# Performance work log

Measured on AMD Instinct MI355X. Metric: run time of the kernel, lower is better.

## Reference

```python
import jax, jax.numpy as jnp
import numpy as np

B, S, D = 2, 2048, 2048
NQ, NKV = 16, 4
HD = D // NQ           # 128
GROUP = NQ // NKV      # 4


def setup_inputs() -> dict:
    key = jax.random.key(0)
    k_x, k_q, k_k, k_v, k_o = jax.random.split(key, 5)
    scale = 0.02
    return {
        "x": jax.random.normal(k_x, (B, S, D), dtype=jnp.float32),
        # torch nn.Linear weights have shape (out_features, in_features)
        "Wq": jax.random.normal(k_q, (D, D), dtype=jnp.float32) * scale,
        "Wk": jax.random.normal(k_k, (NKV * HD, D), dtype=jnp.float32) * scale,
        "Wv": jax.random.normal(k_v, (NKV * HD, D), dtype=jnp.float32) * scale,
        "Wo": jax.random.normal(k_o, (D, D), dtype=jnp.float32) * scale,
    }


def reference(x, Wq, Wk, Wv, Wo):
    b, s, _ = x.shape
    # projections (Linear: x @ W.T), then split heads -> (b, h, s, hd)
    Q = (x @ Wq.T).reshape(b, s, NQ, HD).transpose(0, 2, 1, 3)
    K = (x @ Wk.T).reshape(b, s, NKV, HD).transpose(0, 2, 1, 3)
    V = (x @ Wv.T).reshape(b, s, NKV, HD).transpose(0, 2, 1, 3)
    # GQA: broadcast each KV head across its query-head group (repeat_interleave on head dim)
    K = jnp.repeat(K, GROUP, axis=1)  # (b, NQ, s, hd)
    V = jnp.repeat(V, GROUP, axis=1)
    scores = jnp.einsum("bhqd,bhkd->bhqk", Q, K) / jnp.sqrt(jnp.float32(HD))
    causal = jnp.triu(jnp.ones((s, s), dtype=bool), k=1)  # True above diagonal -> masked
    scores = jnp.where(causal, -jnp.inf, scores)
    weights = jax.nn.softmax(scores, axis=-1)  # dropout p=0.0 -> identity
    ctx = jnp.einsum("bhqk,bhkd->bhqd", weights, V)
    ctx = ctx.transpose(0, 2, 1, 3).reshape(b, s, D)
    return ctx @ Wo.T
```

## Files before the change

kernel.cpp:

```cpp
#include <hip/hip_runtime.h>
#include <stdint.h>

#define S_LEN 2048
#define DMODEL 2048
#define NQH 16
#define NKVH 4
#define HDK 128

typedef __bf16 bf16x8 __attribute__((ext_vector_type(8)));
typedef float f32x4 __attribute__((ext_vector_type(4)));
typedef float f32x16 __attribute__((ext_vector_type(16)));

__device__ __forceinline__ void async16(const void* g, void* l) {
  __builtin_amdgcn_global_load_lds((const __attribute__((address_space(1))) void*)g,
                                   (__attribute__((address_space(3))) void*)l,
                                   16, 0, 0);
}

__device__ __forceinline__ f32x4 mfma16(bf16x8 a, bf16x8 b, f32x4 c) {
  return __builtin_amdgcn_mfma_f32_16x16x32_bf16(a, b, c, 0, 0, 0);
}
__device__ __forceinline__ f32x16 mfma32(bf16x8 a, bf16x8 b, f32x16 c) {
  return __builtin_amdgcn_mfma_f32_32x32x16_bf16(a, b, c, 0, 0, 0);
}
__device__ __forceinline__ uint32_t pkbf16(float lo, float hi) {
  uint32_t r;
  asm("v_cvt_pk_bf16_f32 %0, %1, %2" : "=v"(r) : "v"(lo), "v"(hi));
  return r;
}

__global__ __launch_bounds__(256) void cvt_bf16(const float* __restrict__ in,
                                                __bf16* __restrict__ out, int n) {
  int i = (blockIdx.x * 256 + threadIdx.x) * 8;
  if (i >= n) return;
  const float4* p = (const float4*)(in + i);
  float4 a = p[0], b = p[1];
  bf16x8 o;
  o[0] = (__bf16)a.x; o[1] = (__bf16)a.y; o[2] = (__bf16)a.z; o[3] = (__bf16)a.w;
  o[4] = (__bf16)b.x; o[5] = (__bf16)b.y; o[6] = (__bf16)b.z; o[7] = (__bf16)b.w;
  *(bf16x8*)(out + i) = o;
}

template <bool F32OUT>
__global__ __launch_bounds__(256) void gemm_bt(const __bf16* __restrict__ A,
                                               const __bf16* __restrict__ Ba,
                                               const __bf16* __restrict__ Bb,
                                               void* __restrict__ Ca,
                                               void* __restrict__ Cb,
                                               int M, int Ntot, int Nsplit, int K) {
  int nbn = Ntot >> 7;
  int bx = blockIdx.x;
  int m0 = (bx / nbn) << 7;
  int n0g = (bx % nbn) << 7;
  const __bf16* B;
  void* C;
  int n0, Nc;
  if (n0g < Nsplit) { B = Ba; C = Ca; n0 = n0g; Nc = Nsplit; }
  else              { B = Bb; C = Cb; n0 = n0g - Nsplit; Nc = Ntot - Nsplit; }

  __shared__ __align__(16) uint8_t As[16384];
  __shared__ __align__(16) uint8_t Bs[16384];

  int t = threadIdx.x, lane = t & 63, w = t >> 6;
  int wr = w >> 1, wc = w & 1;
  f32x4 acc[4][4] = {};

  for (int k0 = 0; k0 < K; k0 += 64) {
#pragma unroll
    for (int i = 0; i < 4; ++i) {
      int c = (i << 8) + t;
      int row = c >> 3;
      int colb = ((c & 7) << 4) ^ ((row & 7) << 4);
      async16((const uint8_t*)(A + (size_t)(m0 + row) * K + k0) + colb, As + c * 16);
      async16((const uint8_t*)(B + (size_t)(n0 + row) * K + k0) + colb, Bs + c * 16);
    }
    __syncthreads();
#pragma unroll
    for (int ks = 0; ks < 2; ++ks) {
      bf16x8 af[4], bfr[4];
#pragma unroll
      for (int m = 0; m < 4; ++m) {
        int row = wr * 64 + m * 16 + (lane & 15);
        int colb = ((ks << 6) + ((lane >> 4) << 4)) ^ ((row & 7) << 4);
        af[m] = *(const bf16x8*)(As + row * 128 + colb);
      }
#pragma unroll
      for (int n = 0; n < 4; ++n) {
        int row = wc * 64 + n * 16 + (lane & 15);
        int colb = ((ks << 6) + ((lane >> 4) << 4)) ^ ((row & 7) << 4);
        bfr[n] = *(const bf16x8*)(Bs + row * 128 + colb);
      }
      __builtin_amdgcn_s_setprio(1);
#pragma unroll
      for (int m = 0; m < 4; ++m)
#pragma unroll
        for (int n = 0; n < 4; ++n)
          acc[m][n] = mfma16(af[m], bfr[n], acc[m][n]);
      __builtin_amdgcn_s_setprio(0);
    }
    __syncthreads();
  }
#pragma unroll
  for (int m = 0; m < 4; ++m)
#pragma unroll
    for (int n = 0; n < 4; ++n)
#pragma unroll
      for (int j = 0; j < 4; ++j) {
        int mg = m0 + wr * 64 + m * 16 + ((lane >> 4) << 2) + j;
        int ng = n0 + wc * 64 + n * 16 + (lane & 15);
        float v = acc[m][n][j];
        if (F32OUT) ((float*)C)[(size_t)mg * Nc + ng] = v;
        else        ((__bf16*)C)[(size_t)mg * Nc + ng] = (__bf16)v;
      }
}

__global__ __launch_bounds__(256) void transpose_v(const __bf16* __restrict__ V,
                                                   __bf16* __restrict__ Vt) {
  int bid = blockIdx.x;
  int dt = bid & 1, st = (bid >> 1) & 31, kvh = (bid >> 6) & 3, b = bid >> 8;
  __shared__ __align__(16) __bf16 tile[64][72];
  int t = threadIdx.x;
#pragma unroll
  for (int i = 0; i < 2; ++i) {
    int c = (i << 8) + t;
    int sr = c >> 3, cb = (c & 7) << 3;
    bf16x8 v = *(const bf16x8*)(V + (size_t)(b * S_LEN + st * 64 + sr) * 512 +
                                kvh * HDK + dt * 64 + cb);
    *(bf16x8*)(&tile[sr][cb]) = v;
  }
  __syncthreads();
#pragma unroll
  for (int i = 0; i < 2; ++i) {
    int c = (i << 8) + t;
    int dr = c >> 3, sb = (c & 7) << 3;
    bf16x8 o;
#pragma unroll
    for (int j = 0; j < 8; ++j) o[j] = tile[sb + j][dr];
    *(bf16x8*)(Vt + (size_t)((b * NKVH + kvh) * HDK + dt * 64 + dr) * S_LEN +
               st * 64 + sb) = o;
  }
}

__global__ __launch_bounds__(256, 2) void attn(const __bf16* __restrict__ Q,
                                               const __bf16* __restrict__ Kx,
                                               const __bf16* __restrict__ Vt,
                                               __bf16* __restrict__ Ctx) {
  int bid = blockIdx.x;
  int qt = 15 - (bid & 15);
  int h = (bid >> 4) & 15;
  int b = bid >> 8;
  int kvh = h >> 2;
  int q0 = qt << 7;
  int t = threadIdx.x, lane = t & 63, w = t >> 6;
  int qr = lane & 31;
  int hi = lane >> 5;
  int qwb = q0 + (w << 5);

  __shared__ __align__(16) uint8_t Ks[2][16384];
  __shared__ __align__(16) uint8_t Vs[2][16384];

  const __bf16* kbase = Kx + (size_t)b * S_LEN * 512 + kvh * HDK;
  const __bf16* vbase = Vt + (size_t)(b * NKVH + kvh) * HDK * S_LEN;

  auto stage = [&](int kt, int bufi) {
#pragma unroll
    for (int i = 0; i < 4; ++i) {
      int c = (i << 8) + t;
      int krow = c >> 4;
      int kcolb = ((c & 15) << 4) ^ ((krow & 7) << 4);
      async16((const uint8_t*)(kbase + (size_t)((kt << 6) + krow) * 512) + kcolb,
              Ks[bufi] + c * 16);
      int vrow = c >> 3;
      int vcolb = ((c & 7) << 4) ^ ((vrow & 7) << 4);
      async16((const uint8_t*)(vbase + (size_t)vrow * S_LEN + (kt << 6)) + vcolb,
              Vs[bufi] + c * 16);
    }
  };

  int NT = (qt << 1) + 2;
  stage(0, 0);

  bf16x8 qf[8];
  {
    const __bf16* qrow = Q + (size_t)(b * S_LEN + qwb + qr) * DMODEL + h * HDK + hi * 8;
#pragma unroll
    for (int dk = 0; dk < 8; ++dk) qf[dk] = *(const bf16x8*)(qrow + dk * 16);
  }
  __syncthreads();

  const float NEG = -3.0e38f;
  const float SC = 0.08838834764831845f;
  float m_run = NEG, l_run = 0.f;
  f32x16 acc[4] = {};

  for (int kt = 0; kt < NT; ++kt) {
    int cur = kt & 1;
    if (kt + 1 < NT) stage(kt + 1, cur ^ 1);
    int k0 = kt << 6;
    if (k0 <= qwb + 31) {
      const uint8_t* ks = Ks[cur];
      const uint8_t* vs = Vs[cur];

      f32x16 st0 = {}, st1 = {};
      __builtin_amdgcn_s_setprio(1);
#pragma unroll
      for (int dk = 0; dk < 8; ++dk) {
        int cb = (dk << 5) + (hi << 4);
        int swz = (qr & 7) << 4;
        bf16x8 kf0 = *(const bf16x8*)(ks + qr * 256 + (cb ^ swz));
        st0 = mfma32(kf0, qf[dk], st0);
        bf16x8 kf1 = *(const bf16x8*)(ks + (32 + qr) * 256 + (cb ^ swz));
        st1 = mfma32(kf1, qf[dk], st1);
      }
      __builtin_amdgcn_s_setprio(0);

      if (k0 + 63 > qwb) {
#pragma unroll
        for (int r = 0; r < 16; ++r) {
          int kl = (r & 3) + ((r >> 2) << 3) + (hi << 2);
          st0[r] = (k0 + kl > qwb + qr) ? NEG : st0[r];
          st1[r] = (k0 + 32 + kl > qwb + qr) ? NEG : st1[r];
        }
      }

      float mx = fmaxf(st0[0], st1[0]);
#pragma unroll
      for (int r = 1; r < 16; ++r) mx = fmaxf(mx, fmaxf(st0[r], st1[r]));
      mx = fmaxf(mx, __shfl_xor(mx, 32, 64));

      if (__any(mx > m_run + 90.52f)) {
        float mn = fmaxf(m_run, mx);
        float al = __expf((m_run - mn) * SC);
        l_run *= al;
        m_run = mn;
#pragma unroll
        for (int i = 0; i < 16; ++i) {
          float alr = __shfl(al, (i & 3) + ((i >> 2) << 3) + (hi << 2), 64);
          acc[0][i] *= alr; acc[1][i] *= alr; acc[2][i] *= alr; acc[3][i] *= alr;
        }
      }

      float mSC = m_run * SC;
      float rs = 0.f;
      float p0[16], p1[16];
#pragma unroll
      for (int r = 0; r < 16; ++r) { p0[r] = __expf(fmaf(st0[r], SC, -mSC)); rs += p0[r]; }
#pragma unroll
      for (int r = 0; r < 16; ++r) { p1[r] = __expf(fmaf(st1[r], SC, -mSC)); rs += p1[r]; }
      rs += __shfl_xor(rs, 32, 64);
      l_run += rs;

      uint32_t wd0[4][2], wd1[4][2];
#pragma unroll
      for (int g = 0; g < 4; ++g) {
        wd0[g][0] = pkbf16(p0[4 * g + 0], p0[4 * g + 1]);
        wd0[g][1] = pkbf16(p0[4 * g + 2], p0[4 * g + 3]);
        wd1[g][0] = pkbf16(p1[4 * g + 0], p1[4 * g + 1]);
        wd1[g][1] = pkbf16(p1[4 * g + 2], p1[4 * g + 3]);
      }
      bf16x8 pa[4];
#define PEXCH(WD, IDX0, IDX1)                                                  \
      {                                                                        \
        uint32_t s0 = hi ? WD[0][0] : WD[1][0];                                \
        uint32_t s1 = hi ? WD[0][1] : WD[1][1];                                \
        uint32_t s2 = hi ? WD[2][0] : WD[3][0];                                \
        uint32_t s3 = hi ? WD[2][1] : WD[3][1];                                \
        uint32_t r0 = (uint32_t)__shfl_xor((int)s0, 32, 64);                   \
        uint32_t r1 = (uint32_t)__shfl_xor((int)s1, 32, 64);                   \
        uint32_t r2 = (uint32_t)__shfl_xor((int)s2, 32, 64);                   \
        uint32_t r3 = (uint32_t)__shfl_xor((int)s3, 32, 64);                   \
        union { bf16x8 v; uint32_t u[4]; } fa, fb;                             \
        fa.u[0] = hi ? r0 : WD[0][0];                                          \
        fa.u[1] = hi ? r1 : WD[0][1];                                          \
        fa.u[2] = hi ? WD[1][0] : r0;                                          \
        fa.u[3] = hi ? WD[1][1] : r1;                                          \
        fb.u[0] = hi ? r2 : WD[2][0];                                          \
        fb.u[1] = hi ? r3 : WD[2][1];                                          \
        fb.u[2] = hi ? WD[3][0] : r2;                                          \
        fb.u[3] = hi ? WD[3][1] : r3;                                          \
        pa[IDX0] = fa.v;                                                       \
        pa[IDX1] = fb.v;                                                       \
      }
      PEXCH(wd0, 0, 1)
      PEXCH(wd1, 2, 3)
#undef PEXCH

      __builtin_amdgcn_s_setprio(1);
#pragma unroll
      for (int dt = 0; dt < 4; ++dt) {
        int row = (dt << 5) + qr;
        int swz = (row & 7) << 4;
#pragma unroll
        for (int kc = 0; kc < 4; ++kc) {
          bf16x8 vf = *(const bf16x8*)(vs + row * 128 + (((kc << 5) + (hi << 4)) ^ swz));
          acc[dt] = mfma32(pa[kc], vf, acc[dt]);
        }
      }
      __builtin_amdgcn_s_setprio(0);
    }
    __syncthreads();
  }

#pragma unroll
  for (int i = 0; i < 16; ++i) {
    int rm = (i & 3) + ((i >> 2) << 3) + (hi << 2);
    float lr = __shfl(l_run, rm, 64);
    float inv = 1.0f / lr;
    size_t rowoff = (size_t)(b * S_LEN + qwb + rm) * DMODEL + h * HDK + qr;
#pragma unroll
    for (int dt = 0; dt < 4; ++dt)
      Ctx[rowoff + (dt << 5)] = (__bf16)(acc[dt][i] * inv);
  }
}

extern "C" void kernel_launch(void* const* d_in, const int* in_sizes, int n_in,
                              void* d_out, int out_size, void* d_ws, size_t ws_size,
                              hipStream_t stream) {
  const float* x  = (const float*)d_in[0];
  const float* Wq = (const float*)d_in[1];
  const float* Wk = (const float*)d_in[2];
  const float* Wv = (const float*)d_in[3];
  const float* Wo = (const float*)d_in[4];
  float* out = (float*)d_out;

  const size_t MB = 1024 * 1024;
  uint8_t* ws = (uint8_t*)d_ws;
  __bf16* xb  = (__bf16*)(ws + 0 * MB);
  __bf16* Wqb = (__bf16*)(ws + 16 * MB);
  __bf16* Wkb = (__bf16*)(ws + 24 * MB);
  __bf16* Wvb = (__bf16*)(ws + 26 * MB);
  __bf16* Wob = (__bf16*)(ws + 28 * MB);
  __bf16* Qb  = (__bf16*)(ws + 36 * MB);
  __bf16* Kb  = (__bf16*)(ws + 52 * MB);
  __bf16* Vb  = (__bf16*)(ws + 56 * MB);
  __bf16* Vtb = (__bf16*)(ws + 60 * MB);
  __bf16* Ctx = (__bf16*)(ws + 64 * MB);

  cvt_bf16<<<8388608 / 2048, 256, 0, stream>>>(x, xb, 8388608);
  cvt_bf16<<<4194304 / 2048, 256, 0, stream>>>(Wq, Wqb, 4194304);
  cvt_bf16<<<1048576 / 2048, 256, 0, stream>>>(Wk, Wkb, 1048576);
  cvt_bf16<<<1048576 / 2048, 256, 0, stream>>>(Wv, Wvb, 1048576);
  cvt_bf16<<<4194304 / 2048, 256, 0, stream>>>(Wo, Wob, 4194304);

  gemm_bt<false><<<(4096 / 128) * (2048 / 128), 256, 0, stream>>>(
      xb, Wqb, Wqb, (void*)Qb, (void*)Qb, 4096, 2048, 2048, 2048);
  gemm_bt<false><<<(4096 / 128) * (1024 / 128), 256, 0, stream>>>(
      xb, Wkb, Wvb, (void*)Kb, (void*)Vb, 4096, 1024, 512, 2048);

  transpose_v<<<512, 256, 0, stream>>>(Vb, Vtb);

  attn<<<2 * 16 * 16, 256, 0, stream>>>(Qb, Kb, Vtb, Ctx);

  gemm_bt<true><<<(4096 / 128) * (2048 / 128), 256, 0, stream>>>(
      Ctx, Wob, Wob, (void*)out, (void*)out, 4096, 2048, 2048, 2048);
}
```

Baseline: 233.2 us.

## Fuse conversions and QKV GEMMs, add XCD-aware block remap, tree reductions

Merges the five fp32-to-bf16 conversion launches into one kernel, and the Q and K/V projection GEMMs into a single launch with three output splits. It also remaps block indices in the GEMMs and the attention kernel so that neighbouring tiles are spread across the XCDs. The softmax max and sum reductions inside attention become tree reductions to shorten dependency chains. The aim is to cut launch overhead and tail effects and to improve L2 locality, at the cost of extra branching and index arithmetic.

```diff
diff --git a/kernel.cpp b/kernel.cpp
--- a/kernel.cpp
+++ b/kernel.cpp
@@ -29,10 +29,22 @@
   return r;
 }
 
-__global__ __launch_bounds__(256) void cvt_bf16(const float* __restrict__ in,
-                                                __bf16* __restrict__ out, int n) {
-  int i = (blockIdx.x * 256 + threadIdx.x) * 8;
-  if (i >= n) return;
+__global__ __launch_bounds__(256) void cvt_all(
+    const float* __restrict__ i0, const float* __restrict__ i1,
+    const float* __restrict__ i2, const float* __restrict__ i3,
+    const float* __restrict__ i4, __bf16* __restrict__ o0,
+    __bf16* __restrict__ o1, __bf16* __restrict__ o2, __bf16* __restrict__ o3,
+    __bf16* __restrict__ o4) {
+  int v = blockIdx.x * 256 + threadIdx.x;
+  const float* in;
+  __bf16* out;
+  int base;
+  if (v < 1048576)      { in = i0; out = o0; base = 0; }
+  else if (v < 1572864) { in = i1; out = o1; base = 1048576; }
+  else if (v < 1703936) { in = i2; out = o2; base = 1572864; }
+  else if (v < 1835008) { in = i3; out = o3; base = 1703936; }
+  else                  { in = i4; out = o4; base = 1835008; }
+  int i = (v - base) * 8;
   const float4* p = (const float4*)(in + i);
   float4 a = p[0], b = p[1];
   bf16x8 o;
@@ -43,20 +55,25 @@
 
 template <bool F32OUT>
 __global__ __launch_bounds__(256) void gemm_bt(const __bf16* __restrict__ A,
-                                               const __bf16* __restrict__ Ba,
-                                               const __bf16* __restrict__ Bb,
-                                               void* __restrict__ Ca,
-                                               void* __restrict__ Cb,
-                                               int M, int Ntot, int Nsplit, int K) {
+                                               const __bf16* __restrict__ B0,
+                                               const __bf16* __restrict__ B1,
+                                               const __bf16* __restrict__ B2,
+                                               void* __restrict__ C0,
+                                               void* __restrict__ C1,
+                                               void* __restrict__ C2,
+                                               int Ntot, int Ns1, int Ns2, int K) {
   int nbn = Ntot >> 7;
-  int bx = blockIdx.x;
+  int nwg = gridDim.x;
+  int bid = blockIdx.x;
+  int bx = (bid & 7) * (nwg >> 3) + (bid >> 3);
   int m0 = (bx / nbn) << 7;
   int n0g = (bx % nbn) << 7;
   const __bf16* B;
   void* C;
   int n0, Nc;
-  if (n0g < Nsplit) { B = Ba; C = Ca; n0 = n0g; Nc = Nsplit; }
-  else              { B = Bb; C = Cb; n0 = n0g - Nsplit; Nc = Ntot - Nsplit; }
+  if (n0g < Ns1)      { B = B0; C = C0; n0 = n0g;       Nc = Ns1; }
+  else if (n0g < Ns2) { B = B1; C = C1; n0 = n0g - Ns1; Nc = Ns2 - Ns1; }
+  else                { B = B2; C = C2; n0 = n0g - Ns2; Nc = Ntot - Ns2; }
 
   __shared__ __align__(16) uint8_t As[16384];
   __shared__ __align__(16) uint8_t Bs[16384];
@@ -145,7 +162,8 @@
                                                const __bf16* __restrict__ Kx,
                                                const __bf16* __restrict__ Vt,
                                                __bf16* __restrict__ Ctx) {
-  int bid = blockIdx.x;
+  int bid0 = blockIdx.x;
+  int bid = ((bid0 & 7) << 6) | (bid0 >> 3);
   int qt = 15 - (bid & 15);
   int h = (bid >> 4) & 15;
   int b = bid >> 8;
@@ -223,10 +241,14 @@
         }
       }
 
-      float mx = fmaxf(st0[0], st1[0]);
-#pragma unroll
-      for (int r = 1; r < 16; ++r) mx = fmaxf(mx, fmaxf(st0[r], st1[r]));
-      mx = fmaxf(mx, __shfl_xor(mx, 32, 64));
+      float tm[16];
+#pragma unroll
+      for (int r = 0; r < 16; ++r) tm[r] = fmaxf(st0[r], st1[r]);
+#pragma unroll
+      for (int s = 8; s > 0; s >>= 1)
+#pragma unroll
+        for (int r = 0; r < s; ++r) tm[r] = fmaxf(tm[r], tm[r + s]);
+      float mx = fmaxf(tm[0], __shfl_xor(tm[0], 32, 64));
 
       if (__any(mx > m_run + 90.52f)) {
         float mn = fmaxf(m_run, mx);
@@ -241,14 +263,19 @@
       }
 
       float mSC = m_run * SC;
-      float rs = 0.f;
       float p0[16], p1[16];
 #pragma unroll
-      for (int r = 0; r < 16; ++r) { p0[r] = __expf(fmaf(st0[r], SC, -mSC)); rs += p0[r]; }
-#pragma unroll
-      for (int r = 0; r < 16; ++r) { p1[r] = __expf(fmaf(st1[r], SC, -mSC)); rs += p1[r]; }
-      rs += __shfl_xor(rs, 32, 64);
-      l_run += rs;
+      for (int r = 0; r < 16; ++r) p0[r] = __expf(fmaf(st0[r], SC, -mSC));
+#pragma unroll
+      for (int r = 0; r < 16; ++r) p1[r] = __expf(fmaf(st1[r], SC, -mSC));
+      float ts[16];
+#pragma unroll
+      for (int r = 0; r < 16; ++r) ts[r] = p0[r] + p1[r];
+#pragma unroll
+      for (int s = 8; s > 0; s >>= 1)
+#pragma unroll
+        for (int r = 0; r < s; ++r) ts[r] += ts[r + s];
+      l_run += ts[0] + __shfl_xor(ts[0], 32, 64);
 
       uint32_t wd0[4][2], wd1[4][2];
 #pragma unroll
@@ -336,21 +363,15 @@
   __bf16* Vtb = (__bf16*)(ws + 60 * MB);
   __bf16* Ctx = (__bf16*)(ws + 64 * MB);
 
-  cvt_bf16<<<8388608 / 2048, 256, 0, stream>>>(x, xb, 8388608);
-  cvt_bf16<<<4194304 / 2048, 256, 0, stream>>>(Wq, Wqb, 4194304);
-  cvt_bf16<<<1048576 / 2048, 256, 0, stream>>>(Wk, Wkb, 1048576);
-  cvt_bf16<<<1048576 / 2048, 256, 0, stream>>>(Wv, Wvb, 1048576);
-  cvt_bf16<<<4194304 / 2048, 256, 0, stream>>>(Wo, Wob, 4194304);
-
-  gemm_bt<false><<<(4096 / 128) * (2048 / 128), 256, 0, stream>>>(
-      xb, Wqb, Wqb, (void*)Qb, (void*)Qb, 4096, 2048, 2048, 2048);
-  gemm_bt<false><<<(4096 / 128) * (1024 / 128), 256, 0, stream>>>(
-      xb, Wkb, Wvb, (void*)Kb, (void*)Vb, 4096, 1024, 512, 2048);
+  cvt_all<<<9216, 256, 0, stream>>>(x, Wq, Wk, Wv, Wo, xb, Wqb, Wkb, Wvb, Wob);
+
+  gemm_bt<false><<<(4096 / 128) * (3072 / 128), 256, 0, stream>>>(
+      xb, Wqb, Wkb, Wvb, (void*)Qb, (void*)Kb, (void*)Vb, 3072, 2048, 2560, 2048);
 
   transpose_v<<<512, 256, 0, stream>>>(Vb, Vtb);
 
   attn<<<2 * 16 * 16, 256, 0, stream>>>(Qb, Kb, Vtb, Ctx);
 
   gemm_bt<true><<<(4096 / 128) * (2048 / 128), 256, 0, stream>>>(
-      Ctx, Wob, Wob, (void*)out, (void*)out, 4096, 2048, 2048, 2048);
-}
+      Ctx, Wob, Wob, Wob, (void*)out, (void*)out, (void*)out, 2048, 2048, 2048, 2048);
+}
```

After: 200.1 us. 1.17x faster.
